# Optimization experiments

Hardware: AMD Instinct MI355X
Metric: run time of the kernel (lower is better)

## Reference

```python
import jax, jax.numpy as jnp
import numpy as np

VOCAB = 200000
EDIM = 256
R = 16


def setup_inputs() -> dict:
    key = jax.random.key(0)
    k0, k1, k2 = jax.random.split(key, 3)
    x = jax.random.randint(k0, (4096, 50), 0, VOCAB)
    # TR cores: core0 (r1, num_embeddings, r0), core1 (r0, embedding_dim, r1)
    core0 = jax.random.normal(k1, (R, VOCAB, R), dtype=jnp.float32)
    core1 = jax.random.normal(k2, (R, EDIM, R), dtype=jnp.float32)
    return {"x": x, "core0": core0, "core1": core1}


def reference(x, core0, core1):
    # tr_to_tensor for 2 cores: weight[i, j] = trace(core0[:, i, :] @ core1[:, j, :])
    # core0: (a=r1, i=vocab, b=r0), core1: (b=r0, j=edim, a=r1)
    weight = jnp.einsum('aib,bja->ij', core0, core1)  # [vocab, edim]
    return weight[x]  # gather: [batch, hist, edim]
```

## Files before the change

### kernel.cpp

```cpp
#include <hip/hip_runtime.h>
#include <hip/hip_bf16.h>

#define VOCAB  200000
#define NTILES 12800
#define GRID   512
#define ITERS  25
#define DEPTH  3

typedef __attribute__((ext_vector_type(4))) float  f32x4;
typedef __attribute__((ext_vector_type(4))) int    i32x4;
typedef __attribute__((ext_vector_type(8))) __bf16 bf16x8;

typedef const __attribute__((address_space(1))) unsigned int* gas_u32p;
typedef __attribute__((address_space(3))) unsigned int* las_u32p;

__device__ __forceinline__ __bf16 f2bf(float f) {
    unsigned u = __builtin_bit_cast(unsigned, f);
    u += 0x7FFFu + ((u >> 16) & 1u);
    unsigned short s = (unsigned short)(u >> 16);
    return __builtin_bit_cast(__bf16, s);
}

__global__ void pack_b_kernel(const float* __restrict__ core1, bf16x8* __restrict__ bpk) {
    int t    = blockIdx.x * 256 + threadIdx.x;
    int lane = t & 63;
    int nt   = (t >> 6) & 15;
    int kk   = t >> 10;
    int j     = nt * 16 + (lane & 15);
    int kbase = kk * 32 + ((lane >> 4) * 8);
    bf16x8 v;
#pragma unroll
    for (int e = 0; e < 8; ++e) {
        int k = kbase + e;
        int b = k & 15, a = k >> 4;
        v[e] = f2bf(core1[(b * 256 + j) * 16 + a]);
    }
    bpk[t] = v;
}

__device__ __forceinline__ void issue_gather(const float* __restrict__ core0, int idx,
                                             int kk, char* abuf, int lane) {
    const int q = lane >> 4;
#pragma unroll
    for (int h = 0; h < 2; ++h) {
        const float* src = core0 + ((long)(2 * kk + h) * VOCAB + idx) * 16 + q * 4;
        __builtin_amdgcn_global_load_lds((gas_u32p)src,
                                         (las_u32p)(abuf + kk * 2048 + h * 1024), 16, 0, 0);
    }
}

__global__ __launch_bounds__(512, 4) void tr_embed_kernel(
        const int* __restrict__ x, const float* __restrict__ core0,
        const bf16x8* __restrict__ bpk, float* __restrict__ out) {
    __shared__ char lds[DEPTH * 16384 + ITERS * 16 * 4];
    char* const ldsA = lds;
    int*  const sIdx = (int*)(lds + DEPTH * 16384);
    const int tid  = threadIdx.x;
    const int lane = tid & 63;
    const int wave = tid >> 6;
    const int r    = lane & 15;
    const int q    = lane >> 4;
    const int laneOff = q * 512 + r * 16;

    bf16x8 B0[8], B1[8];
#pragma unroll
    for (int kk = 0; kk < 8; ++kk) {
        B0[kk] = bpk[(kk * 16 + 2 * wave)     * 64 + lane];
        B1[kk] = bpk[(kk * 16 + 2 * wave + 1) * 64 + lane];
    }

    const int b0 = blockIdx.x;

    for (int j = tid; j < ITERS * 16; j += 512)
        sIdx[j] = x[(b0 + (j >> 4) * GRID) * 16 + (j & 15)];
    __syncthreads();

#pragma unroll
    for (int p = 0; p < 2; ++p)
        issue_gather(core0, sIdx[p * 16 + r], wave, ldsA + p * 16384, lane);
    asm volatile("s_waitcnt vmcnt(0)" ::: "memory");
    __builtin_amdgcn_s_barrier();
    __builtin_amdgcn_sched_barrier(0);

    int slot = 0;
    for (int i = 0; i < ITERS; ++i) {
        const int t = b0 + i * GRID;
        char* cur = ldsA + slot * 16384;

        if (i + 2 < ITERS) {
            int ns = slot + 2; if (ns >= DEPTH) ns -= DEPTH;
            issue_gather(core0, sIdx[(i + 2) * 16 + r], wave, ldsA + ns * 16384, lane);
        }
        __builtin_amdgcn_sched_barrier(0);

        f32x4 acc0 = {}, acc1 = {};
#pragma unroll
        for (int kk = 0; kk < 8; ++kk) {
            f32x4 lo = *(const f32x4*)(cur + kk * 2048 + laneOff);
            f32x4 hi = *(const f32x4*)(cur + kk * 2048 + laneOff + 256);
            int p0, p1, p2, p3;
            asm("v_cvt_pk_bf16_f32 %0, %1, %2" : "=v"(p0) : "v"(lo[0]), "v"(lo[1]));
            asm("v_cvt_pk_bf16_f32 %0, %1, %2" : "=v"(p1) : "v"(lo[2]), "v"(lo[3]));
            asm("v_cvt_pk_bf16_f32 %0, %1, %2" : "=v"(p2) : "v"(hi[0]), "v"(hi[1]));
            asm("v_cvt_pk_bf16_f32 %0, %1, %2" : "=v"(p3) : "v"(hi[2]), "v"(hi[3]));
            i32x4 pk = { p0, p1, p2, p3 };
            bf16x8 af = __builtin_bit_cast(bf16x8, pk);
            acc0 = __builtin_amdgcn_mfma_f32_16x16x32_bf16(af, B0[kk], acc0, 0, 0, 0);
            acc1 = __builtin_amdgcn_mfma_f32_16x16x32_bf16(af, B1[kk], acc1, 0, 0, 0);
        }

        float* ob = out + (long)t * 16 * 256 + (q * 4) * 256 + 2 * wave * 16 + r;
#pragma unroll
        for (int e = 0; e < 4; ++e) {
            ob[e * 256]      = acc0[e];
            ob[e * 256 + 16] = acc1[e];
        }

        asm volatile("s_waitcnt vmcnt(16)" ::: "memory");
        __builtin_amdgcn_s_barrier();
        __builtin_amdgcn_sched_barrier(0);

        slot = (slot == DEPTH - 1) ? 0 : slot + 1;
    }
}

extern "C" void kernel_launch(void* const* d_in, const int* in_sizes, int n_in,
                              void* d_out, int out_size, void* d_ws, size_t ws_size,
                              hipStream_t stream) {
    const int*   x     = (const int*)d_in[0];
    const float* core0 = (const float*)d_in[1];
    const float* core1 = (const float*)d_in[2];
    float* out = (float*)d_out;
    bf16x8* bpk = (bf16x8*)d_ws;

    pack_b_kernel<<<32, 256, 0, stream>>>(core1, bpk);
    tr_embed_kernel<<<GRID, 512, 0, stream>>>(x, core0, bpk, out);
}
```

Measured before the change: 108.1 us.

## Pre-convert core0 to a bf16 gather-friendly layout before the embedding kernel

Adds a repack kernel that converts the whole core0 table to bf16. It lays the table out so each vocab row is 512 contiguous bytes. The main kernel then gathers half the bytes per lookup with one 16-byte load per lane and drops the in-loop fp32-to-bf16 conversion. The cost is a full pass over the 200k-row table on every call: about 205MB read and 100MB written, paid before any gather. This path runs only when the workspace is large enough; otherwise the old kernel is used.

```diff
diff --git a/kernel.cpp b/kernel.cpp
--- a/kernel.cpp
+++ b/kernel.cpp
@@ -36,6 +36,114 @@
         v[e] = f2bf(core1[(b * 256 + j) * 16 + a]);
     }
     bpk[t] = v;
+}
+
+__global__ __launch_bounds__(256) void repack_a_kernel(const float* __restrict__ core0,
+                                                       char* __restrict__ wbf) {
+    int t = blockIdx.x * 256 + threadIdx.x;
+    int v = t >> 3, j = t & 7;
+    const float* s0 = core0 + ((long)(2 * j)     * VOCAB + v) * 16;
+    const float* s1 = core0 + ((long)(2 * j + 1) * VOCAB + v) * 16;
+    f32x4 a0 = *(const f32x4*)(s0),     a1 = *(const f32x4*)(s0 + 4);
+    f32x4 a2 = *(const f32x4*)(s0 + 8), a3 = *(const f32x4*)(s0 + 12);
+    f32x4 b0 = *(const f32x4*)(s1),     b1 = *(const f32x4*)(s1 + 4);
+    f32x4 b2 = *(const f32x4*)(s1 + 8), b3 = *(const f32x4*)(s1 + 12);
+    int p[16];
+    asm("v_cvt_pk_bf16_f32 %0, %1, %2" : "=v"(p[0])  : "v"(a0[0]), "v"(a0[1]));
+    asm("v_cvt_pk_bf16_f32 %0, %1, %2" : "=v"(p[1])  : "v"(a0[2]), "v"(a0[3]));
+    asm("v_cvt_pk_bf16_f32 %0, %1, %2" : "=v"(p[2])  : "v"(a1[0]), "v"(a1[1]));
+    asm("v_cvt_pk_bf16_f32 %0, %1, %2" : "=v"(p[3])  : "v"(a1[2]), "v"(a1[3]));
+    asm("v_cvt_pk_bf16_f32 %0, %1, %2" : "=v"(p[4])  : "v"(a2[0]), "v"(a2[1]));
+    asm("v_cvt_pk_bf16_f32 %0, %1, %2" : "=v"(p[5])  : "v"(a2[2]), "v"(a2[3]));
+    asm("v_cvt_pk_bf16_f32 %0, %1, %2" : "=v"(p[6])  : "v"(a3[0]), "v"(a3[1]));
+    asm("v_cvt_pk_bf16_f32 %0, %1, %2" : "=v"(p[7])  : "v"(a3[2]), "v"(a3[3]));
+    asm("v_cvt_pk_bf16_f32 %0, %1, %2" : "=v"(p[8])  : "v"(b0[0]), "v"(b0[1]));
+    asm("v_cvt_pk_bf16_f32 %0, %1, %2" : "=v"(p[9])  : "v"(b0[2]), "v"(b0[3]));
+    asm("v_cvt_pk_bf16_f32 %0, %1, %2" : "=v"(p[10]) : "v"(b1[0]), "v"(b1[1]));
+    asm("v_cvt_pk_bf16_f32 %0, %1, %2" : "=v"(p[11]) : "v"(b1[2]), "v"(b1[3]));
+    asm("v_cvt_pk_bf16_f32 %0, %1, %2" : "=v"(p[12]) : "v"(b2[0]), "v"(b2[1]));
+    asm("v_cvt_pk_bf16_f32 %0, %1, %2" : "=v"(p[13]) : "v"(b2[2]), "v"(b2[3]));
+    asm("v_cvt_pk_bf16_f32 %0, %1, %2" : "=v"(p[14]) : "v"(b3[0]), "v"(b3[1]));
+    asm("v_cvt_pk_bf16_f32 %0, %1, %2" : "=v"(p[15]) : "v"(b3[2]), "v"(b3[3]));
+    char* dst = wbf + (long)v * 512 + j * 64;
+    i32x4 o0 = { p[0], p[1], p[2], p[3] };
+    i32x4 o1 = { p[4], p[5], p[6], p[7] };
+    i32x4 o2 = { p[8], p[9], p[10], p[11] };
+    i32x4 o3 = { p[12], p[13], p[14], p[15] };
+    *(i32x4*)(dst)      = o0;  *(i32x4*)(dst + 16) = o1;
+    *(i32x4*)(dst + 32) = o2;  *(i32x4*)(dst + 48) = o3;
+}
+
+__device__ __forceinline__ void issue_gather_bf(const char* __restrict__ wbf, int idx,
+                                                int wave, int q, char* abuf) {
+    const char* src = wbf + (long)idx * 512 + wave * 64 + q * 16;
+    __builtin_amdgcn_global_load_lds((gas_u32p)src, (las_u32p)(abuf + wave * 1024), 16, 0, 0);
+}
+
+__global__ __launch_bounds__(512, 4) void tr_embed_bf_kernel(
+        const int* __restrict__ x, const char* __restrict__ wbf,
+        const bf16x8* __restrict__ bpk, float* __restrict__ out) {
+    __shared__ char lds[DEPTH * 8192 + ITERS * 16 * 4];
+    char* const ldsA = lds;
+    int*  const sIdx = (int*)(lds + DEPTH * 8192);
+    const int tid  = threadIdx.x;
+    const int lane = tid & 63;
+    const int wave = tid >> 6;
+    const int r    = lane & 15;
+    const int q    = lane >> 4;
+
+    bf16x8 B0[8], B1[8];
+#pragma unroll
+    for (int kk = 0; kk < 8; ++kk) {
+        B0[kk] = bpk[(kk * 16 + 2 * wave)     * 64 + lane];
+        B1[kk] = bpk[(kk * 16 + 2 * wave + 1) * 64 + lane];
+    }
+
+    const int b0 = blockIdx.x;
+
+    for (int j = tid; j < ITERS * 16; j += 512)
+        sIdx[j] = x[(b0 + (j >> 4) * GRID) * 16 + (j & 15)];
+    __syncthreads();
+
+#pragma unroll
+    for (int p = 0; p < 2; ++p)
+        issue_gather_bf(wbf, sIdx[p * 16 + r], wave, q, ldsA + p * 8192);
+    asm volatile("s_waitcnt vmcnt(0)" ::: "memory");
+    __builtin_amdgcn_s_barrier();
+    __builtin_amdgcn_sched_barrier(0);
+
+    int slot = 0;
+    for (int i = 0; i < ITERS; ++i) {
+        const int t = b0 + i * GRID;
+        char* cur = ldsA + slot * 8192;
+
+        if (i + 2 < ITERS) {
+            int ns = slot + 2; if (ns >= DEPTH) ns -= DEPTH;
+            issue_gather_bf(wbf, sIdx[(i + 2) * 16 + r], wave, q, ldsA + ns * 8192);
+        }
+        __builtin_amdgcn_sched_barrier(0);
+
+        f32x4 acc0 = {}, acc1 = {};
+#pragma unroll
+        for (int kk = 0; kk < 8; ++kk) {
+            bf16x8 af = *(const bf16x8*)(cur + kk * 1024 + lane * 16);
+            acc0 = __builtin_amdgcn_mfma_f32_16x16x32_bf16(af, B0[kk], acc0, 0, 0, 0);
+            acc1 = __builtin_amdgcn_mfma_f32_16x16x32_bf16(af, B1[kk], acc1, 0, 0, 0);
+        }
+
+        float* ob = out + (long)t * 16 * 256 + (q * 4) * 256 + 2 * wave * 16 + r;
+#pragma unroll
+        for (int e = 0; e < 4; ++e) {
+            ob[e * 256]      = acc0[e];
+            ob[e * 256 + 16] = acc1[e];
+        }
+
+        asm volatile("s_waitcnt vmcnt(16)" ::: "memory");
+        __builtin_amdgcn_s_barrier();
+        __builtin_amdgcn_sched_barrier(0);
+
+        slot = (slot == DEPTH - 1) ? 0 : slot + 1;
+    }
 }
 
 __device__ __forceinline__ void issue_gather(const float* __restrict__ core0, int idx,
@@ -70,7 +178,6 @@
     }
 
     const int b0 = blockIdx.x;
-
     for (int j = tid; j < ITERS * 16; j += 512)
         sIdx[j] = x[(b0 + (j >> 4) * GRID) * 16 + (j & 15)];
     __syncthreads();
@@ -86,7 +193,6 @@
     for (int i = 0; i < ITERS; ++i) {
         const int t = b0 + i * GRID;
         char* cur = ldsA + slot * 16384;
-
         if (i + 2 < ITERS) {
             int ns = slot + 2; if (ns >= DEPTH) ns -= DEPTH;
             issue_gather(core0, sIdx[(i + 2) * 16 + r], wave, ldsA + ns * 16384, lane);
@@ -115,11 +221,9 @@
             ob[e * 256]      = acc0[e];
             ob[e * 256 + 16] = acc1[e];
         }
-
         asm volatile("s_waitcnt vmcnt(16)" ::: "memory");
         __builtin_amdgcn_s_barrier();
         __builtin_amdgcn_sched_barrier(0);
-
         slot = (slot == DEPTH - 1) ? 0 : slot + 1;
     }
 }
@@ -132,7 +236,15 @@
     const float* core1 = (const float*)d_in[2];
     float* out = (float*)d_out;
     bf16x8* bpk = (bf16x8*)d_ws;
+    char*   wbf = (char*)d_ws + 131072;
+
+    const size_t WS_NEED = 131072 + (size_t)VOCAB * 512;
 
     pack_b_kernel<<<32, 256, 0, stream>>>(core1, bpk);
-    tr_embed_kernel<<<GRID, 512, 0, stream>>>(x, core0, bpk, out);
-}
+    if (ws_size >= WS_NEED) {
+        repack_a_kernel<<<VOCAB * 8 / 256, 256, 0, stream>>>(core0, wbf);
+        tr_embed_bf_kernel<<<GRID, 512, 0, stream>>>(x, wbf, bpk, out);
+    } else {
+        tr_embed_kernel<<<GRID, 512, 0, stream>>>(x, core0, bpk, out);
+    }
+}
```

Measured after the change: 150.9 us. 39.6% more time.

## Bucket-sort token indices by vocab region before gather for locality

Applied to the files above, without the earlier changes.

Adds a counting sort (histogram, scan, atomic scatter) that groups the 204800 token positions by index>>4 and builds a permutation. The embed kernel then processes tokens in sorted order, so gathers from core0 hit nearby rows and get better cache reuse. Output rows are staged through swizzled LDS and written as contiguous 1KB rows to their permuted destinations. This adds four small kernels, a single-block scan, and global atomics in exchange for gather locality.

```diff
diff --git a/kernel.cpp b/kernel.cpp
--- a/kernel.cpp
+++ b/kernel.cpp
@@ -2,10 +2,12 @@
 #include <hip/hip_bf16.h>
 
 #define VOCAB  200000
+#define NROWS  204800
 #define NTILES 12800
 #define GRID   512
 #define ITERS  25
 #define DEPTH  3
+#define NBUCK  12500
 
 typedef __attribute__((ext_vector_type(4))) float  f32x4;
 typedef __attribute__((ext_vector_type(4))) int    i32x4;
@@ -38,6 +40,44 @@
     bpk[t] = v;
 }
 
+__global__ void zero_hist_kernel(int* __restrict__ hist) {
+    int t = blockIdx.x * 1024 + threadIdx.x;
+    if (t < 13312) hist[t] = 0;
+}
+
+__global__ void hist_kernel(const int* __restrict__ x, int* __restrict__ hist) {
+    int i = blockIdx.x * 1024 + threadIdx.x;
+    atomicAdd(&hist[x[i] >> 4], 1);
+}
+
+__global__ __launch_bounds__(1024) void scan_kernel(const int* __restrict__ hist,
+                                                    int* __restrict__ basec) {
+    __shared__ int ps[1024];
+    const int tt = threadIdx.x;
+    const int c0 = tt * 13;
+    int part = 0;
+#pragma unroll
+    for (int k = 0; k < 13; ++k) { int b = c0 + k; if (b < NBUCK) part += hist[b]; }
+    ps[tt] = part; __syncthreads();
+    for (int off = 1; off < 1024; off <<= 1) {
+        int v = (tt >= off) ? ps[tt - off] : 0; __syncthreads();
+        ps[tt] += v; __syncthreads();
+    }
+    int run = ps[tt] - part;
+#pragma unroll
+    for (int k = 0; k < 13; ++k) {
+        int b = c0 + k;
+        if (b < NBUCK) { basec[b] = run; run += hist[b]; }
+    }
+}
+
+__global__ void scatter_kernel(const int* __restrict__ x, int* __restrict__ basec,
+                               int* __restrict__ perm) {
+    int i = blockIdx.x * 1024 + threadIdx.x;
+    int pos = atomicAdd(&basec[x[i] >> 4], 1);
+    perm[pos] = i;
+}
+
 __device__ __forceinline__ void issue_gather(const float* __restrict__ core0, int idx,
                                              int kk, char* abuf, int lane) {
     const int q = lane >> 4;
@@ -46,6 +86,101 @@
         const float* src = core0 + ((long)(2 * kk + h) * VOCAB + idx) * 16 + q * 4;
         __builtin_amdgcn_global_load_lds((gas_u32p)src,
                                          (las_u32p)(abuf + kk * 2048 + h * 1024), 16, 0, 0);
+    }
+}
+
+__global__ __launch_bounds__(512, 4) void tr_embed_sorted_kernel(
+        const int* __restrict__ x, const float* __restrict__ core0,
+        const bf16x8* __restrict__ bpk, const int* __restrict__ perm,
+        float* __restrict__ out) {
+    __shared__ char lds[DEPTH * 16384 + 16384 + 400 * 4 + 400 * 4];
+    char* const ldsA = lds;
+    char* const ldsC = lds + DEPTH * 16384;
+    int*  const sIdx  = (int*)(lds + DEPTH * 16384 + 16384);
+    int*  const sPerm = sIdx + 400;
+    const int tid  = threadIdx.x;
+    const int lane = tid & 63;
+    const int wave = tid >> 6;
+    const int r    = lane & 15;
+    const int q    = lane >> 4;
+    const int laneOff = q * 512 + r * 16;
+
+    bf16x8 B0[8], B1[8];
+#pragma unroll
+    for (int kk = 0; kk < 8; ++kk) {
+        B0[kk] = bpk[(kk * 16 + 2 * wave)     * 64 + lane];
+        B1[kk] = bpk[(kk * 16 + 2 * wave + 1) * 64 + lane];
+    }
+
+    const int b0 = blockIdx.x;
+
+    for (int j = tid; j < 400; j += 512) {
+        int p = perm[b0 * 400 + j];
+        sPerm[j] = p;
+        sIdx[j]  = x[p];
+    }
+    __syncthreads();
+
+#pragma unroll
+    for (int p = 0; p < 2; ++p)
+        issue_gather(core0, sIdx[p * 16 + r], wave, ldsA + p * 16384, lane);
+    asm volatile("s_waitcnt vmcnt(0)" ::: "memory");
+    __builtin_amdgcn_s_barrier();
+    __builtin_amdgcn_sched_barrier(0);
+
+    int slot = 0;
+    for (int i = 0; i < ITERS; ++i) {
+        char* cur = ldsA + slot * 16384;
+
+        if (i + 2 < ITERS) {
+            int ns = slot + 2; if (ns >= DEPTH) ns -= DEPTH;
+            issue_gather(core0, sIdx[(i + 2) * 16 + r], wave, ldsA + ns * 16384, lane);
+        }
+        __builtin_amdgcn_sched_barrier(0);
+
+        f32x4 acc0 = {}, acc1 = {};
+#pragma unroll
+        for (int kk = 0; kk < 8; ++kk) {
+            f32x4 lo = *(const f32x4*)(cur + kk * 2048 + laneOff);
+            f32x4 hi = *(const f32x4*)(cur + kk * 2048 + laneOff + 256);
+            int p0, p1, p2, p3;
+            asm("v_cvt_pk_bf16_f32 %0, %1, %2" : "=v"(p0) : "v"(lo[0]), "v"(lo[1]));
+            asm("v_cvt_pk_bf16_f32 %0, %1, %2" : "=v"(p1) : "v"(lo[2]), "v"(lo[3]));
+            asm("v_cvt_pk_bf16_f32 %0, %1, %2" : "=v"(p2) : "v"(hi[0]), "v"(hi[1]));
+            asm("v_cvt_pk_bf16_f32 %0, %1, %2" : "=v"(p3) : "v"(hi[2]), "v"(hi[3]));
+            i32x4 pk = { p0, p1, p2, p3 };
+            bf16x8 af = __builtin_bit_cast(bf16x8, pk);
+            acc0 = __builtin_amdgcn_mfma_f32_16x16x32_bf16(af, B0[kk], acc0, 0, 0, 0);
+            acc1 = __builtin_amdgcn_mfma_f32_16x16x32_bf16(af, B1[kk], acc1, 0, 0, 0);
+        }
+
+#pragma unroll
+        for (int e = 0; e < 4; ++e) {
+            int row = q * 4 + e;
+            int xr  = (row & 7) << 2;
+            *(float*)(ldsC + row * 1024 + (((2 * wave * 16 + r)      ^ xr) << 2)) = acc0[e];
+            *(float*)(ldsC + row * 1024 + (((2 * wave * 16 + 16 + r) ^ xr) << 2)) = acc1[e];
+        }
+        asm volatile("s_waitcnt lgkmcnt(0)" ::: "memory");
+        __builtin_amdgcn_sched_barrier(0);
+        __builtin_amdgcn_s_barrier();
+        __builtin_amdgcn_sched_barrier(0);
+
+        {
+            int r0w = 2 * wave, r1w = 2 * wave + 1;
+            int row0 = sPerm[i * 16 + r0w];
+            int row1 = sPerm[i * 16 + r1w];
+            f32x4 v0 = *(const f32x4*)(ldsC + r0w * 1024 + (((lane * 4) ^ ((r0w & 7) << 2)) << 2));
+            f32x4 v1 = *(const f32x4*)(ldsC + r1w * 1024 + (((lane * 4) ^ ((r1w & 7) << 2)) << 2));
+            *((f32x4*)(out + (long)row0 * 256) + lane) = v0;
+            *((f32x4*)(out + (long)row1 * 256) + lane) = v1;
+        }
+
+        asm volatile("s_waitcnt vmcnt(4)" ::: "memory");
+        __builtin_amdgcn_s_barrier();
+        __builtin_amdgcn_sched_barrier(0);
+
+        slot = (slot == DEPTH - 1) ? 0 : slot + 1;
     }
 }
 
@@ -70,7 +205,6 @@
     }
 
     const int b0 = blockIdx.x;
-
     for (int j = tid; j < ITERS * 16; j += 512)
         sIdx[j] = x[(b0 + (j >> 4) * GRID) * 16 + (j & 15)];
     __syncthreads();
@@ -86,7 +220,6 @@
     for (int i = 0; i < ITERS; ++i) {
         const int t = b0 + i * GRID;
         char* cur = ldsA + slot * 16384;
-
         if (i + 2 < ITERS) {
             int ns = slot + 2; if (ns >= DEPTH) ns -= DEPTH;
             issue_gather(core0, sIdx[(i + 2) * 16 + r], wave, ldsA + ns * 16384, lane);
@@ -115,11 +248,9 @@
             ob[e * 256]      = acc0[e];
             ob[e * 256 + 16] = acc1[e];
         }
-
         asm volatile("s_waitcnt vmcnt(16)" ::: "memory");
         __builtin_amdgcn_s_barrier();
         __builtin_amdgcn_sched_barrier(0);
-
         slot = (slot == DEPTH - 1) ? 0 : slot + 1;
     }
 }
@@ -131,8 +262,21 @@
     const float* core0 = (const float*)d_in[1];
     const float* core1 = (const float*)d_in[2];
     float* out = (float*)d_out;
-    bf16x8* bpk = (bf16x8*)d_ws;
+
+    bf16x8* bpk   = (bf16x8*)d_ws;
+    int*    hist  = (int*)((char*)d_ws + 131072);
+    int*    basec = (int*)((char*)d_ws + 184320);
+    int*    perm  = (int*)((char*)d_ws + 237568);
+    const size_t WS_NEED = 237568 + (size_t)NROWS * 4;
 
     pack_b_kernel<<<32, 256, 0, stream>>>(core1, bpk);
-    tr_embed_kernel<<<GRID, 512, 0, stream>>>(x, core0, bpk, out);
-}
+    if (ws_size >= WS_NEED) {
+        zero_hist_kernel<<<13, 1024, 0, stream>>>(hist);
+        hist_kernel<<<NROWS / 1024, 1024, 0, stream>>>(x, hist);
+        scan_kernel<<<1, 1024, 0, stream>>>(hist, basec);
+        scatter_kernel<<<NROWS / 1024, 1024, 0, stream>>>(x, basec, perm);
+        tr_embed_sorted_kernel<<<GRID, 512, 0, stream>>>(x, core0, bpk, perm, out);
+    } else {
+        tr_embed_kernel<<<GRID, 512, 0, stream>>>(x, core0, bpk, out);
+    }
+}
```

After: 131.5 us. 1.22x slower.
